# Optimization experiments

Measured on AMD Instinct MI355X. Metric: run time of the kernel, lower is better.

Reference implementation:

```python
import jax, jax.numpy as jnp
import numpy as np

B, Z, TDIM, CF, A, R, T = 1024, 256, 512, 1024, 64, 128, 64

def _lstm_cell(x, h, c, Wih, Whh, b):
    # PyTorch gate order: i, f, g, o
    g = x @ Wih.T + h @ Whh.T + b
    i, f, gg, o = jnp.split(g, 4, axis=-1)
    c = jax.nn.sigmoid(f) * c + jax.nn.sigmoid(i) * jnp.tanh(gg)
    h = jax.nn.sigmoid(o) * jnp.tanh(c)
    return h, c

def setup_inputs() -> dict:
    key = jax.random.key(0)
    ks = jax.random.split(key, 24)
    s = lambda k, shape, fan: jax.random.normal(k, shape, jnp.float32) * (1.0 / np.sqrt(fan))
    d = {}
    d['z'] = jax.random.normal(ks[0], (B, Z), jnp.float32)
    d['z2t_w'] = s(ks[1], (TDIM, Z), Z)
    d['z2t_b'] = jnp.zeros((TDIM,), jnp.float32)
    in_a, in_r, in_t = TDIM + A, TDIM + A + R, TDIM + A + 1
    d['Wih_a'] = s(ks[2], (4 * CF, in_a), in_a); d['Whh_a'] = s(ks[3], (4 * CF, CF), CF); d['b_a'] = jnp.zeros((4 * CF,), jnp.float32)
    d['Wih_r'] = s(ks[4], (4 * CF, in_r), in_r); d['Whh_r'] = s(ks[5], (4 * CF, CF), CF); d['b_r'] = jnp.zeros((4 * CF,), jnp.float32)
    d['Wih_t'] = s(ks[6], (4 * CF, in_t), in_t); d['Whh_t'] = s(ks[7], (4 * CF, CF), CF); d['b_t'] = jnp.zeros((4 * CF,), jnp.float32)
    d['e2act_w'] = s(ks[8], (A, CF), CF); d['e2act_b'] = jnp.zeros((A,), jnp.float32)
    d['e2res_w'] = s(ks[9], (R, CF), CF); d['e2res_b'] = jnp.zeros((R,), jnp.float32)
    d['e2ts_w1'] = s(ks[10], (CF // 2, CF), CF); d['e2ts_b1'] = jnp.zeros((CF // 2,), jnp.float32)
    d['e2ts_w2'] = s(ks[11], (1, CF // 2), CF // 2); d['e2ts_b2'] = jnp.zeros((1,), jnp.float32)
    return d

def reference(z, z2t_w, z2t_b, Wih_a, Whh_a, b_a, Wih_r, Whh_r, b_r, Wih_t, Whh_t, b_t,
              e2act_w, e2act_b, e2res_w, e2res_b, e2ts_w1, e2ts_b1, e2ts_w2, e2ts_b2):
    t_rec = jax.nn.relu(z @ z2t_w.T + z2t_b)                  # [B, TDIM]
    b = t_rec.shape[0]
    act_oh = jnp.tile(jax.nn.one_hot(A - 1, A, dtype=jnp.float32), (b, 1))   # EOT activity
    res_oh = jnp.tile(jax.nn.one_hot(R - 1, R, dtype=jnp.float32), (b, 1))   # EOT resource
    ts_v = jnp.zeros((b, 1), jnp.float32)
    zeros_h = jnp.zeros((b, CF), jnp.float32)
    carry0 = (act_oh, res_oh, ts_v, zeros_h, zeros_h, zeros_h, zeros_h, zeros_h, zeros_h)

    def step(carry, _):
        act_oh, res_oh, ts_v, ha, ca, hr, cr, ht, ct = carry
        xa = jnp.concatenate([t_rec, act_oh], axis=-1)
        ha, ca = _lstm_cell(xa, ha, ca, Wih_a, Whh_a, b_a)
        act_logits = ha @ e2act_w.T + e2act_b                 # [B, A]
        act_oh2 = jax.nn.one_hot(jnp.argmax(act_logits, axis=-1), A, dtype=jnp.float32)
        xr = jnp.concatenate([t_rec, act_oh2, res_oh], axis=-1)
        hr, cr = _lstm_cell(xr, hr, cr, Wih_r, Whh_r, b_r)
        res_logits = hr @ e2res_w.T + e2res_b                 # [B, R]
        res_oh2 = jax.nn.one_hot(jnp.argmax(res_logits, axis=-1), R, dtype=jnp.float32)
        xt = jnp.concatenate([t_rec, act_oh2, ts_v], axis=-1)
        ht, ct = _lstm_cell(xt, ht, ct, Wih_t, Whh_t, b_t)
        ts_new = jax.nn.relu(ht @ e2ts_w1.T + e2ts_b1) @ e2ts_w2.T + e2ts_b2  # [B, 1]
        new_carry = (act_oh2, res_oh2, ts_new, ha, ca, hr, cr, ht, ct)
        return new_carry, (act_logits, res_logits, ts_new)

    _, (act_seq, res_seq, ts_seq) = jax.lax.scan(step, carry0, None, length=T)
    acts_rec = jax.nn.softmax(jnp.transpose(act_seq, (1, 0, 2)), axis=2)   # [B, T, A]
    ress_rec = jax.nn.softmax(jnp.transpose(res_seq, (1, 0, 2)), axis=2)   # [B, T, R]
    ts_rec = jnp.transpose(ts_seq[..., 0], (1, 0))                         # [B, T]
    return acts_rec, ts_rec, ress_rec
```

## Files before the change

kernel.cpp:

```cpp
#include <hip/hip_runtime.h>
#include <math.h>


__device__ __forceinline__ float sigf(float x) { return 1.0f / (1.0f + expf(-x)); }

typedef __attribute__((ext_vector_type(8))) _Float16 f16x8;
typedef __attribute__((ext_vector_type(4))) float f32x4;

__device__ __forceinline__ void split_f16(float x, unsigned short& hi, unsigned short& lo) {
    _Float16 h = (_Float16)x;
    float r = (x - (float)h) * 2048.0f;
    _Float16 l = (_Float16)r;
    hi = __builtin_bit_cast(unsigned short, h);
    lo = __builtin_bit_cast(unsigned short, l);
}

#define GLDS(gp, lp) __builtin_amdgcn_global_load_lds( \
    (const __attribute__((address_space(1))) void*)(gp), \
    (__attribute__((address_space(3))) void*)(lp), 16, 0, 0)

__global__ __launch_bounds__(256) void step1(
    const unsigned short* __restrict__ Ah, const unsigned short* __restrict__ Al,
    const unsigned short* __restrict__ WA0, const unsigned short* __restrict__ WA1,
    const float* __restrict__ base_a, const float* __restrict__ Ea, const int* __restrict__ aidx,
    float* __restrict__ ca, unsigned short* __restrict__ oAh, unsigned short* __restrict__ oAl,
    float* __restrict__ haf,
    const unsigned short* __restrict__ Th, const unsigned short* __restrict__ Tl,
    const unsigned short* __restrict__ W10, const unsigned short* __restrict__ W11,
    const float* __restrict__ b1, float* __restrict__ u,
    const float* __restrict__ hrf, const float* __restrict__ resT4, const float* __restrict__ resb,
    float* __restrict__ out_res, int* __restrict__ ridx, int t, int Loff)
{
    int L = blockIdx.x + Loff;
    if (L >= 576) {
        if (t == 0) return;
        int lane = threadIdx.x & 63, w = threadIdx.x >> 6;
        int b = (L - 576) * 4 + w;
        float acc0 = resb[lane], acc1 = resb[lane + 64];
        const float4* arow = (const float4*)(hrf + (size_t)b * 1024);
#pragma unroll 4
        for (int k4 = 0; k4 < 256; k4++) {
            float4 a4 = arow[k4];
            float4 w40 = *(const float4*)(resT4 + ((size_t)k4 * 128 + lane) * 4);
            float4 w41 = *(const float4*)(resT4 + ((size_t)k4 * 128 + lane + 64) * 4);
            acc0 += a4.x * w40.x + a4.y * w40.y + a4.z * w40.z + a4.w * w40.w;
            acc1 += a4.x * w41.x + a4.y * w41.y + a4.z * w41.z + a4.w * w41.w;
        }
        float v = acc0; int idx = lane;
        if (acc1 > v) { v = acc1; idx = lane + 64; }
#pragma unroll
        for (int off = 32; off; off >>= 1) {
            float ov = __shfl_xor(v, off);
            int   oi = __shfl_xor(idx, off);
            if (ov > v || (ov == v && oi < idx)) { v = ov; idx = oi; }
        }
        float e0 = expf(acc0 - v), e1 = expf(acc1 - v);
        float s = e0 + e1;
#pragma unroll
        for (int off = 32; off; off >>= 1) s += __shfl_xor(s, off);
        float* dst = out_res + ((size_t)b * 64 + (t - 1)) * 128;
        dst[lane] = e0 / s; dst[lane + 64] = e1 / s;
        if (lane == 0) ridx[b] = idx;
        return;
    }

    __shared__ unsigned short lds[24576];
    const unsigned short *pAh, *pAl, *pWh, *pWl;
    int x, jy; bool isA;
    if (L < 512) {
        isA = true;
        int xcd = L & 7, idx = L >> 3;
        jy = xcd * 8 + (idx >> 3);
        x = idx & 7;
        pAh = Ah; pAl = Al; pWh = WA0; pWl = WA1;
    } else {
        isA = false;
        int t2 = L - 512;
        x = t2 & 7; jy = t2 >> 3;
        pAh = Th; pAl = Tl; pWh = W10; pWl = W11;
    }
    const int tid = threadIdx.x, wave = tid >> 6, lane = tid & 63;
    const int lrow = lane & 15, lq = lane >> 4;
    const int m0 = x * 128;

    f32x4 acch[2][4], accl[2][4];
#pragma unroll
    for (int i = 0; i < 2; i++)
#pragma unroll
        for (int j = 0; j < 4; j++) {
            acch[i][j] = (f32x4){0.f, 0.f, 0.f, 0.f};
            accl[i][j] = (f32x4){0.f, 0.f, 0.f, 0.f};
        }

    const int nrow = isA ? (wave * 1024 + jy * 16 + lrow) : (jy * 64 + wave * 16 + lrow);

    auto STAGE = [&](int it, int p) {
        int k = it * 32 + lq * 8;
        unsigned short* bp = &lds[p * 12288];
#pragma unroll
        for (int ss = 0; ss < 2; ss++) {
            int s = wave * 2 + ss;
            int mrow = m0 + s * 16 + lrow;
            GLDS(pAh + (size_t)mrow * 1024 + k, bp + s * 512);
            GLDS(pAl + (size_t)mrow * 1024 + k, bp + 4096 + s * 512);
        }
        GLDS(pWh + (size_t)nrow * 1024 + k, bp + 8192 + wave * 512);
        GLDS(pWl + (size_t)nrow * 1024 + k, bp + 10240 + wave * 512);
    };
    auto COMPUTE = [&](int p) {
        unsigned short* bp = &lds[p * 12288];
        f16x8 ah[2], al[2], bh[4], bl[4];
#pragma unroll
        for (int mi = 0; mi < 2; mi++) {
            ah[mi] = *(const f16x8*)(bp + (wave * 2 + mi) * 512 + lane * 8);
            al[mi] = *(const f16x8*)(bp + 4096 + (wave * 2 + mi) * 512 + lane * 8);
        }
#pragma unroll
        for (int ni = 0; ni < 4; ni++) {
            bh[ni] = *(const f16x8*)(bp + 8192 + ni * 512 + lane * 8);
            bl[ni] = *(const f16x8*)(bp + 10240 + ni * 512 + lane * 8);
        }
#pragma unroll
        for (int mi = 0; mi < 2; mi++)
#pragma unroll
            for (int ni = 0; ni < 4; ni++) {
                acch[mi][ni] = __builtin_amdgcn_mfma_f32_16x16x32_f16(ah[mi], bh[ni], acch[mi][ni], 0, 0, 0);
                accl[mi][ni] = __builtin_amdgcn_mfma_f32_16x16x32_f16(al[mi], bh[ni], accl[mi][ni], 0, 0, 0);
                accl[mi][ni] = __builtin_amdgcn_mfma_f32_16x16x32_f16(ah[mi], bl[ni], accl[mi][ni], 0, 0, 0);
            }
    };

    STAGE(0, 0);
    for (int it = 0; it < 31; ++it) {
        int cur = it & 1;
        STAGE(it + 1, cur ^ 1);
        asm volatile("s_waitcnt vmcnt(6)" ::: "memory");
        __builtin_amdgcn_s_barrier();
        __builtin_amdgcn_sched_barrier(0);
        COMPUTE(cur);
        __builtin_amdgcn_sched_barrier(0);
        __builtin_amdgcn_s_barrier();
    }
    asm volatile("s_waitcnt vmcnt(0)" ::: "memory");
    __builtin_amdgcn_s_barrier();
    __builtin_amdgcn_sched_barrier(0);
    COMPUTE(1);

    const float s_lo = 1.0f / 2048.0f;
    if (isA) {
        int j = jy * 16 + lrow;
#pragma unroll
        for (int mi = 0; mi < 2; mi++)
#pragma unroll
            for (int r = 0; r < 4; r++) {
                int row = m0 + wave * 32 + mi * 16 + lq * 4 + r;
                size_t rb = (size_t)row * 4096 + j;
                const float* e1 = Ea + (size_t)aidx[row] * 4096 + j;
                float gi = acch[mi][0][r] + accl[mi][0][r] * s_lo + base_a[rb]        + e1[0];
                float gf = acch[mi][1][r] + accl[mi][1][r] * s_lo + base_a[rb + 1024] + e1[1024];
                float gg = acch[mi][2][r] + accl[mi][2][r] * s_lo + base_a[rb + 2048] + e1[2048];
                float go = acch[mi][3][r] + accl[mi][3][r] * s_lo + base_a[rb + 3072] + e1[3072];
                size_t ci = (size_t)row * 1024 + j;
                float cn = sigf(gf) * ca[ci] + sigf(gi) * tanhf(gg);
                ca[ci] = cn;
                float hn = sigf(go) * tanhf(cn);
                haf[ci] = hn;
                split_f16(hn, oAh[ci], oAl[ci]);
            }
    } else {
#pragma unroll
        for (int mi = 0; mi < 2; mi++)
#pragma unroll
            for (int ni = 0; ni < 4; ni++) {
                int col = jy * 64 + ni * 16 + lrow;
                float bv = b1[col];
#pragma unroll
                for (int r = 0; r < 4; r++) {
                    int row = m0 + wave * 32 + mi * 16 + lq * 4 + r;
                    float v = acch[mi][ni][r] + accl[mi][ni][r] * s_lo + bv;
                    u[(size_t)row * 512 + col] = fmaxf(v, 0.0f);
                }
            }
    }
}

__global__ __launch_bounds__(256) void step3(
    const unsigned short* __restrict__ Rh, const unsigned short* __restrict__ Rl,
    const unsigned short* __restrict__ WR0, const unsigned short* __restrict__ WR1,
    const float* __restrict__ base_r, const float* __restrict__ Er_a, const float* __restrict__ Er_r,
    const int* __restrict__ aidx, const int* __restrict__ ridx, const float* __restrict__ tsv,
    float* __restrict__ cr, unsigned short* __restrict__ oRh, unsigned short* __restrict__ oRl,
    float* __restrict__ hrf,
    const unsigned short* __restrict__ Th, const unsigned short* __restrict__ Tl,
    const unsigned short* __restrict__ WT0, const unsigned short* __restrict__ WT1,
    const float* __restrict__ base_t, const float* __restrict__ Et_a, const float* __restrict__ wtts,
    float* __restrict__ ct, unsigned short* __restrict__ oTh, unsigned short* __restrict__ oTl)
{
    __shared__ unsigned short lds[24576];
    int L = blockIdx.x;
    int xcd = L & 7, idx = L >> 3;
    int g = xcd * 16 + (idx >> 3);
    int x = idx & 7;
    int z = g >> 6, jy = g & 63;
    const unsigned short* pAh = z ? Th : Rh;
    const unsigned short* pAl = z ? Tl : Rl;
    const unsigned short* pWh = z ? WT0 : WR0;
    const unsigned short* pWl = z ? WT1 : WR1;

    const int tid = threadIdx.x, wave = tid >> 6, lane = tid & 63;
    const int lrow = lane & 15, lq = lane >> 4;
    const int m0 = x * 128;

    f32x4 acch[2][4], accl[2][4];
#pragma unroll
    for (int i = 0; i < 2; i++)
#pragma unroll
        for (int j = 0; j < 4; j++) {
            acch[i][j] = (f32x4){0.f, 0.f, 0.f, 0.f};
            accl[i][j] = (f32x4){0.f, 0.f, 0.f, 0.f};
        }

    const int nrow = wave * 1024 + jy * 16 + lrow;

    auto STAGE = [&](int it, int p) {
        int k = it * 32 + lq * 8;
        unsigned short* bp = &lds[p * 12288];
#pragma unroll
        for (int ss = 0; ss < 2; ss++) {
            int s = wave * 2 + ss;
            int mrow = m0 + s * 16 + lrow;
            GLDS(pAh + (size_t)mrow * 1024 + k, bp + s * 512);
            GLDS(pAl + (size_t)mrow * 1024 + k, bp + 4096 + s * 512);
        }
        GLDS(pWh + (size_t)nrow * 1024 + k, bp + 8192 + wave * 512);
        GLDS(pWl + (size_t)nrow * 1024 + k, bp + 10240 + wave * 512);
    };
    auto COMPUTE = [&](int p) {
        unsigned short* bp = &lds[p * 12288];
        f16x8 ah[2], al[2], bh[4], bl[4];
#pragma unroll
        for (int mi = 0; mi < 2; mi++) {
            ah[mi] = *(const f16x8*)(bp + (wave * 2 + mi) * 512 + lane * 8);
            al[mi] = *(const f16x8*)(bp + 4096 + (wave * 2 + mi) * 512 + lane * 8);
        }
#pragma unroll
        for (int ni = 0; ni < 4; ni++) {
            bh[ni] = *(const f16x8*)(bp + 8192 + ni * 512 + lane * 8);
            bl[ni] = *(const f16x8*)(bp + 10240 + ni * 512 + lane * 8);
        }
#pragma unroll
        for (int mi = 0; mi < 2; mi++)
#pragma unroll
            for (int ni = 0; ni < 4; ni++) {
                acch[mi][ni] = __builtin_amdgcn_mfma_f32_16x16x32_f16(ah[mi], bh[ni], acch[mi][ni], 0, 0, 0);
                accl[mi][ni] = __builtin_amdgcn_mfma_f32_16x16x32_f16(al[mi], bh[ni], accl[mi][ni], 0, 0, 0);
                accl[mi][ni] = __builtin_amdgcn_mfma_f32_16x16x32_f16(ah[mi], bl[ni], accl[mi][ni], 0, 0, 0);
            }
    };

    STAGE(0, 0);
    for (int it = 0; it < 31; ++it) {
        int cur = it & 1;
        STAGE(it + 1, cur ^ 1);
        asm volatile("s_waitcnt vmcnt(6)" ::: "memory");
        __builtin_amdgcn_s_barrier();
        __builtin_amdgcn_sched_barrier(0);
        COMPUTE(cur);
        __builtin_amdgcn_sched_barrier(0);
        __builtin_amdgcn_s_barrier();
    }
    asm volatile("s_waitcnt vmcnt(0)" ::: "memory");
    __builtin_amdgcn_s_barrier();
    __builtin_amdgcn_sched_barrier(0);
    COMPUTE(1);

    const float s_lo = 1.0f / 2048.0f;
    const int j = jy * 16 + lrow;
    if (z == 0) {
#pragma unroll
        for (int mi = 0; mi < 2; mi++)
#pragma unroll
            for (int r = 0; r < 4; r++) {
                int row = m0 + wave * 32 + mi * 16 + lq * 4 + r;
                size_t rb = (size_t)row * 4096 + j;
                const float* e1 = Er_a + (size_t)aidx[row] * 4096 + j;
                const float* e2 = Er_r + (size_t)ridx[row] * 4096 + j;
                float gi = acch[mi][0][r] + accl[mi][0][r] * s_lo + base_r[rb]        + e1[0]    + e2[0];
                float gf = acch[mi][1][r] + accl[mi][1][r] * s_lo + base_r[rb + 1024] + e1[1024] + e2[1024];
                float gg = acch[mi][2][r] + accl[mi][2][r] * s_lo + base_r[rb + 2048] + e1[2048] + e2[2048];
                float go = acch[mi][3][r] + accl[mi][3][r] * s_lo + base_r[rb + 3072] + e1[3072] + e2[3072];
                size_t ci = (size_t)row * 1024 + j;
                float cn = sigf(gf) * cr[ci] + sigf(gi) * tanhf(gg);
                cr[ci] = cn;
                float hn = sigf(go) * tanhf(cn);
                hrf[ci] = hn;
                split_f16(hn, oRh[ci], oRl[ci]);
            }
    } else {
#pragma unroll
        for (int mi = 0; mi < 2; mi++)
#pragma unroll
            for (int r = 0; r < 4; r++) {
                int row = m0 + wave * 32 + mi * 16 + lq * 4 + r;
                size_t rb = (size_t)row * 4096 + j;
                const float* e1 = Et_a + (size_t)aidx[row] * 4096 + j;
                float tv = tsv[row];
                float gi = acch[mi][0][r] + accl[mi][0][r] * s_lo + base_t[rb]        + e1[0];
                float gf = acch[mi][1][r] + accl[mi][1][r] * s_lo + base_t[rb + 1024] + e1[1024];
                float gg = acch[mi][2][r] + accl[mi][2][r] * s_lo + base_t[rb + 2048] + e1[2048];
                float go = acch[mi][3][r] + accl[mi][3][r] * s_lo + base_t[rb + 3072] + e1[3072];
                gi = fmaf(tv, wtts[j], gi);        gf = fmaf(tv, wtts[j + 1024], gf);
                gg = fmaf(tv, wtts[j + 2048], gg); go = fmaf(tv, wtts[j + 3072], go);
                size_t ci = (size_t)row * 1024 + j;
                float cn = sigf(gf) * ct[ci] + sigf(gi) * tanhf(gg);
                ct[ci] = cn;
                float hn = sigf(go) * tanhf(cn);
                split_f16(hn, oTh[ci], oTl[ci]);
            }
    }
}

__global__ __launch_bounds__(256) void heads(
    const float* __restrict__ haf, const float* __restrict__ actT4, const float* __restrict__ actb,
    float* __restrict__ out_acts, int* __restrict__ aidx, int tact,
    const float* __restrict__ u, const float* __restrict__ w2, const float* __restrict__ b2,
    float* __restrict__ out_ts, float* __restrict__ tsv, int tts)
{
    int blk = blockIdx.x;
    int lane = threadIdx.x & 63, w = threadIdx.x >> 6;
    if (blk < 256) {
        if (tact < 0) return;
        int b = blk * 4 + w;
        float acc = actb[lane];
        const float4* arow = (const float4*)(haf + (size_t)b * 1024);
#pragma unroll 4
        for (int k4 = 0; k4 < 256; k4++) {
            float4 a4 = arow[k4];
            float4 w4 = *(const float4*)(actT4 + ((size_t)k4 * 64 + lane) * 4);
            acc += a4.x * w4.x + a4.y * w4.y + a4.z * w4.z + a4.w * w4.w;
        }
        float v = acc; int idx = lane;
#pragma unroll
        for (int off = 32; off; off >>= 1) {
            float ov = __shfl_xor(v, off);
            int   oi = __shfl_xor(idx, off);
            if (ov > v || (ov == v && oi < idx)) { v = ov; idx = oi; }
        }
        float e = expf(acc - v);
        float s = e;
#pragma unroll
        for (int off = 32; off; off >>= 1) s += __shfl_xor(s, off);
        out_acts[((size_t)b * 64 + tact) * 64 + lane] = e / s;
        if (lane == 0) aidx[b] = idx;
    } else {
        if (tts < 0) return;
        int b = (blk - 256) * 4 + w;
        const float* ur = u + (size_t)b * 512;
        float s = 0.0f;
#pragma unroll
        for (int q = 0; q < 8; q++) s = fmaf(ur[lane + q * 64], w2[lane + q * 64], s);
#pragma unroll
        for (int off = 32; off; off >>= 1) s += __shfl_xor(s, off);
        if (lane == 0) {
            float r = s + b2[0];
            out_ts[b * 64 + tts] = r;
            tsv[b] = r;
        }
    }
}

__global__ __launch_bounds__(256) void gemm_f32(
    const float* __restrict__ A0, const float* __restrict__ W0, float* __restrict__ C0,
    const float* __restrict__ A1, const float* __restrict__ W1, float* __restrict__ C1,
    int lda, int ldw, int ldc, int K, const float* __restrict__ bias, int relu)
{
    const float* Ap = blockIdx.z ? A1 : A0;
    const float* Wp = blockIdx.z ? W1 : W0;
    float*       Cp = blockIdx.z ? C1 : C0;
    __shared__ float As[16][128];
    __shared__ float Bs[16][64];
    const int tid = threadIdx.x;
    const int m0 = blockIdx.x * 128, n0 = blockIdx.y * 64;
    const int tx = tid & 7, ty = tid >> 3;
    const bool wal = (ldw & 3) == 0;
    float acc[4][8];
#pragma unroll
    for (int i = 0; i < 4; i++)
#pragma unroll
        for (int j = 0; j < 8; j++) acc[i][j] = 0.0f;

    for (int k0 = 0; k0 < K; k0 += 16) {
        __syncthreads();
#pragma unroll
        for (int q = 0; q < 2; q++) {
            int t2 = tid + q * 256;
            int kq = t2 & 3, m = t2 >> 2;
            float4 v = *(const float4*)(Ap + (size_t)(m0 + m) * lda + k0 + kq * 4);
            As[kq * 4 + 0][m] = v.x; As[kq * 4 + 1][m] = v.y;
            As[kq * 4 + 2][m] = v.z; As[kq * 4 + 3][m] = v.w;
        }
        {
            int kq = tid & 3, n = tid >> 2;
            const float* src = Wp + (size_t)(n0 + n) * ldw + k0 + kq * 4;
            float4 v;
            if (wal) v = *(const float4*)src;
            else { v.x = src[0]; v.y = src[1]; v.z = src[2]; v.w = src[3]; }
            Bs[kq * 4 + 0][n] = v.x; Bs[kq * 4 + 1][n] = v.y;
            Bs[kq * 4 + 2][n] = v.z; Bs[kq * 4 + 3][n] = v.w;
        }
        __syncthreads();
#pragma unroll
        for (int k = 0; k < 16; k++) {
            float a4[4], b8[8];
            *(float4*)a4 = *(const float4*)&As[k][ty * 4];
            *(float4*)(b8) = *(const float4*)&Bs[k][tx * 8];
            *(float4*)(b8 + 4) = *(const float4*)&Bs[k][tx * 8 + 4];
#pragma unroll
            for (int i = 0; i < 4; i++)
#pragma unroll
                for (int j = 0; j < 8; j++) acc[i][j] = fmaf(a4[i], b8[j], acc[i][j]);
        }
    }
#pragma unroll
    for (int i = 0; i < 4; i++) {
        int m = m0 + ty * 4 + i;
        float vb[8];
#pragma unroll
        for (int j = 0; j < 8; j++) {
            float v = acc[i][j];
            if (bias) v += bias[n0 + tx * 8 + j];
            if (relu) v = fmaxf(v, 0.0f);
            vb[j] = v;
        }
        float* dst = Cp + (size_t)m * ldc + n0 + tx * 8;
        *(float4*)dst = make_float4(vb[0], vb[1], vb[2], vb[3]);
        *(float4*)(dst + 4) = make_float4(vb[4], vb[5], vb[6], vb[7]);
    }
}

__global__ void extract_cols(const float* __restrict__ Wih, int ldw, int col0, int ncols,
                             float* __restrict__ E)
{
    int i = blockIdx.x * 256 + threadIdx.x;
    if (i >= ncols * 4096) return;
    int c = i % ncols, j = i / ncols;
    E[(size_t)c * 4096 + j] = Wih[(size_t)j * ldw + col0 + c];
}

__global__ void split_mat_h(const float* __restrict__ X,
                            unsigned short* __restrict__ hi, unsigned short* __restrict__ lo, int n)
{
    int i = blockIdx.x * 256 + threadIdx.x;
    if (i >= n) return;
    split_f16(X[i], hi[i], lo[i]);
}

__global__ void transpose_pack(const float* __restrict__ W, int K, int C, float* __restrict__ out)
{
    int i = blockIdx.x * 256 + threadIdx.x;
    if (i >= C * K) return;
    int c = i / K, k = i - c * K;
    out[(((size_t)(k >> 2) * C + c) << 2) + (k & 3)] = W[i];
}

__global__ void init_state(float* __restrict__ cc, unsigned int* __restrict__ hilo,
                           float* __restrict__ tsv, int* __restrict__ aidx, int* __restrict__ ridx)
{
    int i = blockIdx.x * 256 + threadIdx.x;
    if (i < 3 * 1024 * 1024) cc[i] = 0.0f;
    if (i < 6 * 1024 * 1024) hilo[i] = 0u;
    if (i < 1024) { tsv[i] = 0.0f; aidx[i] = 63; ridx[i] = 127; }
}

extern "C" void kernel_launch(void* const* d_in, const int* in_sizes, int n_in,
                              void* d_out, int out_size, void* d_ws, size_t ws_size,
                              hipStream_t stream)
{
    const float* z       = (const float*)d_in[0];
    const float* z2t_w   = (const float*)d_in[1];
    const float* z2t_b   = (const float*)d_in[2];
    const float* Wih_a   = (const float*)d_in[3];
    const float* Whh_a   = (const float*)d_in[4];
    const float* b_a     = (const float*)d_in[5];
    const float* Wih_r   = (const float*)d_in[6];
    const float* Whh_r   = (const float*)d_in[7];
    const float* b_r     = (const float*)d_in[8];
    const float* Wih_t   = (const float*)d_in[9];
    const float* Whh_t   = (const float*)d_in[10];
    const float* b_t     = (const float*)d_in[11];
    const float* e2act_w = (const float*)d_in[12];
    const float* e2act_b = (const float*)d_in[13];
    const float* e2res_w = (const float*)d_in[14];
    const float* e2res_b = (const float*)d_in[15];
    const float* e2ts_w1 = (const float*)d_in[16];
    const float* e2ts_b1 = (const float*)d_in[17];
    const float* e2ts_w2 = (const float*)d_in[18];
    const float* e2ts_b2 = (const float*)d_in[19];

    float* out_acts = (float*)d_out;
    float* out_ts   = out_acts + (size_t)1024 * 64 * 64;
    float* out_res  = out_ts + 1024 * 64;

    float* ws = (float*)d_ws;
    size_t off = 0;
    auto alloc = [&](size_t n) { float* p = ws + off; off += n; return p; };
    float* t_rec  = alloc((size_t)1024 * 512);
    float* base_a = alloc((size_t)1024 * 4096);
    float* base_r = alloc((size_t)1024 * 4096);
    float* base_t = alloc((size_t)1024 * 4096);
    float* Ea     = alloc((size_t)64 * 4096);
    float* Er_a   = alloc((size_t)64 * 4096);
    float* Er_r   = alloc((size_t)128 * 4096);
    float* Et_a   = alloc((size_t)64 * 4096);
    float* wtts   = alloc(4096);
    float* cc     = alloc((size_t)3 * 1024 * 1024);
    float* ca = cc, * cr = cc + 1048576, * ct = cc + 2097152;
    float* haf    = alloc((size_t)1024 * 1024);
    float* hrf    = alloc((size_t)1024 * 1024);
    float* u      = alloc((size_t)1024 * 512);
    float* tsv    = alloc(1024);
    int*   aidx   = (int*)alloc(1024);
    int*   ridx   = (int*)alloc(1024);
    float* actT4  = alloc((size_t)64 * 1024);
    float* resT4  = alloc((size_t)128 * 1024);
    unsigned short* hilo = (unsigned short*)alloc((size_t)6 * 1024 * 1024);
    const size_t U = 1048576;
    unsigned short* haSp0[2] = {hilo,         hilo + U};
    unsigned short* haSp1[2] = {hilo + 2 * U, hilo + 3 * U};
    unsigned short* hrSp0[2] = {hilo + 4 * U, hilo + 5 * U};
    unsigned short* hrSp1[2] = {hilo + 6 * U, hilo + 7 * U};
    unsigned short* htSp0[2] = {hilo + 8 * U, hilo + 9 * U};
    unsigned short* htSp1[2] = {hilo + 10 * U, hilo + 11 * U};
    unsigned short* WA0 = (unsigned short*)alloc((size_t)2 * 1024 * 1024);
    unsigned short* WA1 = (unsigned short*)alloc((size_t)2 * 1024 * 1024);
    unsigned short* WR0 = (unsigned short*)alloc((size_t)2 * 1024 * 1024);
    unsigned short* WR1 = (unsigned short*)alloc((size_t)2 * 1024 * 1024);
    unsigned short* WT0 = (unsigned short*)alloc((size_t)2 * 1024 * 1024);
    unsigned short* WT1 = (unsigned short*)alloc((size_t)2 * 1024 * 1024);
    unsigned short* W10 = (unsigned short*)alloc((size_t)256 * 1024);
    unsigned short* W11 = (unsigned short*)alloc((size_t)256 * 1024);

    dim3 blk(256);
    init_state<<<(6 * 1024 * 1024 + 255) / 256, blk, 0, stream>>>(cc, (unsigned int*)hilo, tsv, aidx, ridx);

    gemm_f32<<<dim3(8, 8, 1), blk, 0, stream>>>(z, z2t_w, t_rec, z, z2t_w, t_rec,
                                                256, 256, 512, 256, z2t_b, 1);
    gemm_f32<<<dim3(8, 64, 1), blk, 0, stream>>>(t_rec, Wih_a, base_a, t_rec, Wih_a, base_a,
                                                 512, 576, 4096, 512, b_a, 0);
    gemm_f32<<<dim3(8, 64, 1), blk, 0, stream>>>(t_rec, Wih_r, base_r, t_rec, Wih_r, base_r,
                                                 512, 704, 4096, 512, b_r, 0);
    gemm_f32<<<dim3(8, 64, 1), blk, 0, stream>>>(t_rec, Wih_t, base_t, t_rec, Wih_t, base_t,
                                                 512, 577, 4096, 512, b_t, 0);
    extract_cols<<<(64 * 4096 + 255) / 256, blk, 0, stream>>>(Wih_a, 576, 512, 64, Ea);
    extract_cols<<<(64 * 4096 + 255) / 256, blk, 0, stream>>>(Wih_r, 704, 512, 64, Er_a);
    extract_cols<<<(128 * 4096 + 255) / 256, blk, 0, stream>>>(Wih_r, 704, 576, 128, Er_r);
    extract_cols<<<(64 * 4096 + 255) / 256, blk, 0, stream>>>(Wih_t, 577, 512, 64, Et_a);
    extract_cols<<<(4096 + 255) / 256, blk, 0, stream>>>(Wih_t, 577, 576, 1, wtts);
    transpose_pack<<<(64 * 1024 + 255) / 256, blk, 0, stream>>>(e2act_w, 1024, 64, actT4);
    transpose_pack<<<(128 * 1024 + 255) / 256, blk, 0, stream>>>(e2res_w, 1024, 128, resT4);
    split_mat_h<<<(4194304 + 255) / 256, blk, 0, stream>>>(Whh_a, WA0, WA1, 4194304);
    split_mat_h<<<(4194304 + 255) / 256, blk, 0, stream>>>(Whh_r, WR0, WR1, 4194304);
    split_mat_h<<<(4194304 + 255) / 256, blk, 0, stream>>>(Whh_t, WT0, WT1, 4194304);
    split_mat_h<<<(524288 + 255) / 256, blk, 0, stream>>>(e2ts_w1, W10, W11, 524288);

    for (int t = 0; t < 64; t++) {
        int rd = t & 1, wr = rd ^ 1;
        step1<<<832, blk, 0, stream>>>(
            haSp0[rd], haSp1[rd], WA0, WA1, base_a, Ea, aidx,
            ca, haSp0[wr], haSp1[wr], haf,
            htSp0[rd], htSp1[rd], W10, W11, e2ts_b1, u,
            hrf, resT4, e2res_b, out_res, ridx, t, 0);
        heads<<<512, blk, 0, stream>>>(haf, actT4, e2act_b, out_acts, aidx, t,
                                       u, e2ts_w2, e2ts_b2, out_ts, tsv, t - 1);
        step3<<<1024, blk, 0, stream>>>(
            hrSp0[rd], hrSp1[rd], WR0, WR1, base_r, Er_a, Er_r, aidx, ridx, tsv,
            cr, hrSp0[wr], hrSp1[wr], hrf,
            htSp0[rd], htSp1[rd], WT0, WT1, base_t, Et_a, wtts,
            ct, htSp0[wr], htSp1[wr]);
    }
    step1<<<320, blk, 0, stream>>>(
        haSp0[0], haSp1[0], WA0, WA1, base_a, Ea, aidx,
        ca, haSp0[1], haSp1[1], haf,
        htSp0[0], htSp1[0], W10, W11, e2ts_b1, u,
        hrf, resT4, e2res_b, out_res, ridx, 64, 512);
    heads<<<512, blk, 0, stream>>>(haf, actT4, e2act_b, out_acts, aidx, -1,
                                   u, e2ts_w2, e2ts_b2, out_ts, tsv, 63);
}
```

Baseline: 14.51 ms.

## Load A operand directly into registers and stage only weights through LDS

In both GEMM-plus-LSTM kernels, each wave now loads its own hi/lo A fragments from global memory straight into double-buffered registers instead of staging them through LDS. Only the weight (B) tiles still go through LDS via direct global-to-LDS loads. This cuts the LDS footprint from 48KB to 16KB per block, and launch bounds now ask for 4 blocks per CU, to raise occupancy and remove the LDS round trip for A. The cost is higher register pressure and uncoalesced per-lane global reads for A, which now depend on compiler-inserted waits rather than the barrier schedule.

```diff
diff --git a/kernel.cpp b/kernel.cpp
--- a/kernel.cpp
+++ b/kernel.cpp
@@ -19,7 +19,7 @@
     (const __attribute__((address_space(1))) void*)(gp), \
     (__attribute__((address_space(3))) void*)(lp), 16, 0, 0)
 
-__global__ __launch_bounds__(256) void step1(
+__global__ __launch_bounds__(256, 4) void step1(
     const unsigned short* __restrict__ Ah, const unsigned short* __restrict__ Al,
     const unsigned short* __restrict__ WA0, const unsigned short* __restrict__ WA1,
     const float* __restrict__ base_a, const float* __restrict__ Ea, const int* __restrict__ aidx,
@@ -64,7 +64,7 @@
         return;
     }
 
-    __shared__ unsigned short lds[24576];
+    __shared__ unsigned short lds[8192];
     const unsigned short *pAh, *pAl, *pWh, *pWl;
     int x, jy; bool isA;
     if (L < 512) {
@@ -93,58 +93,79 @@
         }
 
     const int nrow = isA ? (wave * 1024 + jy * 16 + lrow) : (jy * 64 + wave * 16 + lrow);
-
-    auto STAGE = [&](int it, int p) {
+    const size_t ar0 = (size_t)(m0 + (wave * 2 + 0) * 16 + lrow) * 1024 + lq * 8;
+    const size_t ar1 = (size_t)(m0 + (wave * 2 + 1) * 16 + lrow) * 1024 + lq * 8;
+
+    f16x8 ah[2][2], al[2][2];
+
+    auto LOADA = [&](int it, int s) {
+        int k = it * 32;
+        ah[s][0] = *(const f16x8*)(pAh + ar0 + k);
+        al[s][0] = *(const f16x8*)(pAl + ar0 + k);
+        ah[s][1] = *(const f16x8*)(pAh + ar1 + k);
+        al[s][1] = *(const f16x8*)(pAl + ar1 + k);
+    };
+    auto STAGEB = [&](int it, int p) {
         int k = it * 32 + lq * 8;
-        unsigned short* bp = &lds[p * 12288];
-#pragma unroll
-        for (int ss = 0; ss < 2; ss++) {
-            int s = wave * 2 + ss;
-            int mrow = m0 + s * 16 + lrow;
-            GLDS(pAh + (size_t)mrow * 1024 + k, bp + s * 512);
-            GLDS(pAl + (size_t)mrow * 1024 + k, bp + 4096 + s * 512);
-        }
-        GLDS(pWh + (size_t)nrow * 1024 + k, bp + 8192 + wave * 512);
-        GLDS(pWl + (size_t)nrow * 1024 + k, bp + 10240 + wave * 512);
+        unsigned short* bp = &lds[p * 4096];
+        GLDS(pWh + (size_t)nrow * 1024 + k, bp + wave * 512);
+        GLDS(pWl + (size_t)nrow * 1024 + k, bp + 2048 + wave * 512);
     };
-    auto COMPUTE = [&](int p) {
-        unsigned short* bp = &lds[p * 12288];
-        f16x8 ah[2], al[2], bh[4], bl[4];
-#pragma unroll
-        for (int mi = 0; mi < 2; mi++) {
-            ah[mi] = *(const f16x8*)(bp + (wave * 2 + mi) * 512 + lane * 8);
-            al[mi] = *(const f16x8*)(bp + 4096 + (wave * 2 + mi) * 512 + lane * 8);
-        }
-#pragma unroll
-        for (int ni = 0; ni < 4; ni++) {
-            bh[ni] = *(const f16x8*)(bp + 8192 + ni * 512 + lane * 8);
-            bl[ni] = *(const f16x8*)(bp + 10240 + ni * 512 + lane * 8);
-        }
-#pragma unroll
-        for (int mi = 0; mi < 2; mi++)
-#pragma unroll
-            for (int ni = 0; ni < 4; ni++) {
-                acch[mi][ni] = __builtin_amdgcn_mfma_f32_16x16x32_f16(ah[mi], bh[ni], acch[mi][ni], 0, 0, 0);
-                accl[mi][ni] = __builtin_amdgcn_mfma_f32_16x16x32_f16(al[mi], bh[ni], accl[mi][ni], 0, 0, 0);
-                accl[mi][ni] = __builtin_amdgcn_mfma_f32_16x16x32_f16(ah[mi], bl[ni], accl[mi][ni], 0, 0, 0);
+    auto COMPUTE = [&](int s, int p) {
+        unsigned short* bp = &lds[p * 4096];
+#pragma unroll
+        for (int nh = 0; nh < 2; nh++) {
+            f16x8 bh[2], bl[2];
+#pragma unroll
+            for (int q = 0; q < 2; q++) {
+                int ni = nh * 2 + q;
+                bh[q] = *(const f16x8*)(bp + ni * 512 + lane * 8);
+                bl[q] = *(const f16x8*)(bp + 2048 + ni * 512 + lane * 8);
             }
+#pragma unroll
+            for (int mi = 0; mi < 2; mi++)
+#pragma unroll
+                for (int q = 0; q < 2; q++) {
+                    int ni = nh * 2 + q;
+                    acch[mi][ni] = __builtin_amdgcn_mfma_f32_16x16x32_f16(ah[s][mi], bh[q], acch[mi][ni], 0, 0, 0);
+                    accl[mi][ni] = __builtin_amdgcn_mfma_f32_16x16x32_f16(al[s][mi], bh[q], accl[mi][ni], 0, 0, 0);
+                    accl[mi][ni] = __builtin_amdgcn_mfma_f32_16x16x32_f16(ah[s][mi], bl[q], accl[mi][ni], 0, 0, 0);
+                }
+        }
     };
 
-    STAGE(0, 0);
-    for (int it = 0; it < 31; ++it) {
-        int cur = it & 1;
-        STAGE(it + 1, cur ^ 1);
-        asm volatile("s_waitcnt vmcnt(6)" ::: "memory");
-        __builtin_amdgcn_s_barrier();
-        __builtin_amdgcn_sched_barrier(0);
-        COMPUTE(cur);
-        __builtin_amdgcn_sched_barrier(0);
-        __builtin_amdgcn_s_barrier();
-    }
+    LOADA(0, 0);
+    STAGEB(0, 0);
+    for (int it = 0; it < 30; it += 2) {
+        STAGEB(it + 1, 1);
+        asm volatile("s_waitcnt vmcnt(2)" ::: "memory");
+        __builtin_amdgcn_s_barrier();
+        __builtin_amdgcn_sched_barrier(0);
+        LOADA(it + 1, 1);
+        COMPUTE(0, 0);
+        __builtin_amdgcn_sched_barrier(0);
+        __builtin_amdgcn_s_barrier();
+        STAGEB(it + 2, 0);
+        asm volatile("s_waitcnt vmcnt(2)" ::: "memory");
+        __builtin_amdgcn_s_barrier();
+        __builtin_amdgcn_sched_barrier(0);
+        LOADA(it + 2, 0);
+        COMPUTE(1, 1);
+        __builtin_amdgcn_sched_barrier(0);
+        __builtin_amdgcn_s_barrier();
+    }
+    STAGEB(31, 1);
+    asm volatile("s_waitcnt vmcnt(2)" ::: "memory");
+    __builtin_amdgcn_s_barrier();
+    __builtin_amdgcn_sched_barrier(0);
+    LOADA(31, 1);
+    COMPUTE(0, 0);
+    __builtin_amdgcn_sched_barrier(0);
+    __builtin_amdgcn_s_barrier();
     asm volatile("s_waitcnt vmcnt(0)" ::: "memory");
     __builtin_amdgcn_s_barrier();
     __builtin_amdgcn_sched_barrier(0);
-    COMPUTE(1);
+    COMPUTE(1, 1);
 
     const float s_lo = 1.0f / 2048.0f;
     if (isA) {
@@ -184,7 +205,7 @@
     }
 }
 
-__global__ __launch_bounds__(256) void step3(
+__global__ __launch_bounds__(256, 4) void step3(
     const unsigned short* __restrict__ Rh, const unsigned short* __restrict__ Rl,
     const unsigned short* __restrict__ WR0, const unsigned short* __restrict__ WR1,
     const float* __restrict__ base_r, const float* __restrict__ Er_a, const float* __restrict__ Er_r,
@@ -196,7 +217,7 @@
     const float* __restrict__ base_t, const float* __restrict__ Et_a, const float* __restrict__ wtts,
     float* __restrict__ ct, unsigned short* __restrict__ oTh, unsigned short* __restrict__ oTl)
 {
-    __shared__ unsigned short lds[24576];
+    __shared__ unsigned short lds[8192];
     int L = blockIdx.x;
     int xcd = L & 7, idx = L >> 3;
     int g = xcd * 16 + (idx >> 3);
@@ -221,58 +242,79 @@
         }
 
     const int nrow = wave * 1024 + jy * 16 + lrow;
-
-    auto STAGE = [&](int it, int p) {
+    const size_t ar0 = (size_t)(m0 + (wave * 2 + 0) * 16 + lrow) * 1024 + lq * 8;
+    const size_t ar1 = (size_t)(m0 + (wave * 2 + 1) * 16 + lrow) * 1024 + lq * 8;
+
+    f16x8 ah[2][2], al[2][2];
+
+    auto LOADA = [&](int it, int s) {
+        int k = it * 32;
+        ah[s][0] = *(const f16x8*)(pAh + ar0 + k);
+        al[s][0] = *(const f16x8*)(pAl + ar0 + k);
+        ah[s][1] = *(const f16x8*)(pAh + ar1 + k);
+        al[s][1] = *(const f16x8*)(pAl + ar1 + k);
+    };
+    auto STAGEB = [&](int it, int p) {
         int k = it * 32 + lq * 8;
-        unsigned short* bp = &lds[p * 12288];
-#pragma unroll
-        for (int ss = 0; ss < 2; ss++) {
-            int s = wave * 2 + ss;
-            int mrow = m0 + s * 16 + lrow;
-            GLDS(pAh + (size_t)mrow * 1024 + k, bp + s * 512);
-            GLDS(pAl + (size_t)mrow * 1024 + k, bp + 4096 + s * 512);
-        }
-        GLDS(pWh + (size_t)nrow * 1024 + k, bp + 8192 + wave * 512);
-        GLDS(pWl + (size_t)nrow * 1024 + k, bp + 10240 + wave * 512);
+        unsigned short* bp = &lds[p * 4096];
+        GLDS(pWh + (size_t)nrow * 1024 + k, bp + wave * 512);
+        GLDS(pWl + (size_t)nrow * 1024 + k, bp + 2048 + wave * 512);
     };
-    auto COMPUTE = [&](int p) {
-        unsigned short* bp = &lds[p * 12288];
-        f16x8 ah[2], al[2], bh[4], bl[4];
-#pragma unroll
-        for (int mi = 0; mi < 2; mi++) {
-            ah[mi] = *(const f16x8*)(bp + (wave * 2 + mi) * 512 + lane * 8);
-            al[mi] = *(const f16x8*)(bp + 4096 + (wave * 2 + mi) * 512 + lane * 8);
-        }
-#pragma unroll
-        for (int ni = 0; ni < 4; ni++) {
-            bh[ni] = *(const f16x8*)(bp + 8192 + ni * 512 + lane * 8);
-            bl[ni] = *(const f16x8*)(bp + 10240 + ni * 512 + lane * 8);
-        }
-#pragma unroll
-        for (int mi = 0; mi < 2; mi++)
-#pragma unroll
-            for (int ni = 0; ni < 4; ni++) {
-                acch[mi][ni] = __builtin_amdgcn_mfma_f32_16x16x32_f16(ah[mi], bh[ni], acch[mi][ni], 0, 0, 0);
-                accl[mi][ni] = __builtin_amdgcn_mfma_f32_16x16x32_f16(al[mi], bh[ni], accl[mi][ni], 0, 0, 0);
-                accl[mi][ni] = __builtin_amdgcn_mfma_f32_16x16x32_f16(ah[mi], bl[ni], accl[mi][ni], 0, 0, 0);
+    auto COMPUTE = [&](int s, int p) {
+        unsigned short* bp = &lds[p * 4096];
+#pragma unroll
+        for (int nh = 0; nh < 2; nh++) {
+            f16x8 bh[2], bl[2];
+#pragma unroll
+            for (int q = 0; q < 2; q++) {
+                int ni = nh * 2 + q;
+                bh[q] = *(const f16x8*)(bp + ni * 512 + lane * 8);
+                bl[q] = *(const f16x8*)(bp + 2048 + ni * 512 + lane * 8);
             }
+#pragma unroll
+            for (int mi = 0; mi < 2; mi++)
+#pragma unroll
+                for (int q = 0; q < 2; q++) {
+                    int ni = nh * 2 + q;
+                    acch[mi][ni] = __builtin_amdgcn_mfma_f32_16x16x32_f16(ah[s][mi], bh[q], acch[mi][ni], 0, 0, 0);
+                    accl[mi][ni] = __builtin_amdgcn_mfma_f32_16x16x32_f16(al[s][mi], bh[q], accl[mi][ni], 0, 0, 0);
+                    accl[mi][ni] = __builtin_amdgcn_mfma_f32_16x16x32_f16(ah[s][mi], bl[q], accl[mi][ni], 0, 0, 0);
+                }
+        }
     };
 
-    STAGE(0, 0);
-    for (int it = 0; it < 31; ++it) {
-        int cur = it & 1;
-        STAGE(it + 1, cur ^ 1);
-        asm volatile("s_waitcnt vmcnt(6)" ::: "memory");
-        __builtin_amdgcn_s_barrier();
-        __builtin_amdgcn_sched_barrier(0);
-        COMPUTE(cur);
-        __builtin_amdgcn_sched_barrier(0);
-        __builtin_amdgcn_s_barrier();
-    }
+    LOADA(0, 0);
+    STAGEB(0, 0);
+    for (int it = 0; it < 30; it += 2) {
+        STAGEB(it + 1, 1);
+        asm volatile("s_waitcnt vmcnt(2)" ::: "memory");
+        __builtin_amdgcn_s_barrier();
+        __builtin_amdgcn_sched_barrier(0);
+        LOADA(it + 1, 1);
+        COMPUTE(0, 0);
+        __builtin_amdgcn_sched_barrier(0);
+        __builtin_amdgcn_s_barrier();
+        STAGEB(it + 2, 0);
+        asm volatile("s_waitcnt vmcnt(2)" ::: "memory");
+        __builtin_amdgcn_s_barrier();
+        __builtin_amdgcn_sched_barrier(0);
+        LOADA(it + 2, 0);
+        COMPUTE(1, 1);
+        __builtin_amdgcn_sched_barrier(0);
+        __builtin_amdgcn_s_barrier();
+    }
+    STAGEB(31, 1);
+    asm volatile("s_waitcnt vmcnt(2)" ::: "memory");
+    __builtin_amdgcn_s_barrier();
+    __builtin_amdgcn_sched_barrier(0);
+    LOADA(31, 1);
+    COMPUTE(0, 0);
+    __builtin_amdgcn_sched_barrier(0);
+    __builtin_amdgcn_s_barrier();
     asm volatile("s_waitcnt vmcnt(0)" ::: "memory");
     __builtin_amdgcn_s_barrier();
     __builtin_amdgcn_sched_barrier(0);
-    COMPUTE(1);
+    COMPUTE(1, 1);
 
     const float s_lo = 1.0f / 2048.0f;
     const int j = jy * 16 + lrow;
```

Result: no change. 14.29 ms (-1.6%).
